# Kernel tuning notes

Measured on AMD Instinct MI355X. Metric: run time of the kernel, lower is better.

The kernel has to match this reference:

```python
import jax
import jax.numpy as jnp
from jax import lax
import numpy as np

# module hyperparameters (match init_kwargs)
IN_C, OUT_C = 32, 64
K, STRIDE, PAD, DIL = 3, 1, 1, 1
GRID_SIZE, ORDER = 5, 3
GRID_LO, GRID_HI = -1.0, 1.0
SCALE_SPLINE = 1.0
EPS = 1e-8


def _knot_grid():
    # grid = arange(-order, grid_size+order+1) * h + lo ; length = grid_size + 2*order + 1 = 12
    h = (GRID_HI - GRID_LO) / GRID_SIZE
    return jnp.arange(-ORDER, GRID_SIZE + ORDER + 1, dtype=jnp.float32) * h + GRID_LO


def _bspline_bases(x):
    """Cox-de Boor recursion. x: (N, P) -> bases: (N, P, GRID_SIZE+ORDER)."""
    grid = _knot_grid()
    xe = x[..., None]  # (N, P, 1)
    bases = ((xe >= grid[:-1]) & (xe < grid[1:])).astype(x.dtype)  # (N, P, 11)
    for k in range(1, ORDER + 1):
        left_den = jnp.maximum(grid[k:-1] - grid[:-(k + 1)], EPS)
        right_den = jnp.maximum(grid[k + 1:] - grid[1:-k], EPS)
        bases = ((xe - grid[:-(k + 1)]) / left_den * bases[..., :-1]
                 + (grid[k + 1:] - xe) / right_den * bases[..., 1:])
    return bases  # (N, P, 8)


def setup_inputs() -> dict:
    key = jax.random.key(0)
    k1, k2, k3 = jax.random.split(key, 3)
    x = jax.random.normal(k1, (4, IN_C, 56, 56), dtype=jnp.float32)
    base_weight = jax.random.normal(k2, (OUT_C, IN_C, K, K), dtype=jnp.float32) * 0.05
    spline_weight = jax.random.normal(k3, (OUT_C, IN_C * K * K, GRID_SIZE + ORDER), dtype=jnp.float32) * 0.05
    spline_scaler = jnp.ones((OUT_C,), dtype=jnp.float32)
    return {"x": x, "base_weight": base_weight,
            "spline_weight": spline_weight, "spline_scaler": spline_scaler}


def reference(x, base_weight, spline_weight, spline_scaler):
    B, C, H, W = x.shape
    pad = [(PAD, PAD), (PAD, PAD)]
    # base path: conv2d -> SiLU
    base_conv = lax.conv_general_dilated(
        x, base_weight, window_strides=(STRIDE, STRIDE), padding=pad,
        rhs_dilation=(DIL, DIL), dimension_numbers=("NCHW", "OIHW", "NCHW"))
    base_out = jax.nn.silu(base_conv)

    # unfold: (B, C*K*K, oh, ow) with torch Unfold channel ordering (c, kh, kw)
    patches = lax.conv_general_dilated_patches(
        x, filter_shape=(K, K), window_strides=(STRIDE, STRIDE), padding=pad,
        rhs_dilation=(DIL, DIL))
    oh, ow = patches.shape[2], patches.shape[3]
    num_patches = oh * ow
    # (B*num_patches, C*K*K)
    pf = patches.reshape(B, C * K * K, num_patches).transpose(0, 2, 1).reshape(-1, C * K * K)

    bases = _bspline_bases(pf)  # (N, P, F)
    # contract patch-dim and basis-dim against spline weights
    spl = jnp.einsum("npf,opf->no", bases, spline_weight) * spline_scaler  # (N, O)
    spl = spl.reshape(B, num_patches, OUT_C).transpose(0, 2, 1).reshape(B, OUT_C, oh, ow)
    return base_out + SCALE_SPLINE * spl
```

## Files before the change

### kernel.cpp

```cpp
#include <hip/hip_runtime.h>
#include <math.h>


typedef __attribute__((ext_vector_type(8))) short bf16x8;
typedef __attribute__((ext_vector_type(4))) float f32x4;

#define MFMA(a, b, c) __builtin_amdgcn_mfma_f32_16x16x32_bf16((a), (b), (c), 0, 0, 0)

__device__ __forceinline__ unsigned short f2bf(float f) {
    unsigned u = __builtin_bit_cast(unsigned, f);
    u = (u + 0x7fffu + ((u >> 16) & 1u)) >> 16;
    return (unsigned short)u;
}

__device__ __forceinline__ void eval_bases(float v, float bs[8]) {
    #pragma unroll
    for (int i = 0; i < 8; ++i) bs[i] = 0.0f;
    float t = (v + 2.2f) * 2.5f;
    if (t >= 0.0f && t < 11.0f) {
        int j = (int)t;
        if (j > 10) j = 10;
        float knot = (float)(j - 3) * 0.4f - 1.0f;
        float u  = (v - knot) * 2.5f;
        float um = 1.0f - u;
        float u2 = u * u, u3 = u2 * u;
        const float s6 = 1.0f / 6.0f;
        float w0 = um * um * um * s6;
        float w1 = (3.0f * u3 - 6.0f * u2 + 4.0f) * s6;
        float w2 = (-3.0f * u3 + 3.0f * u2 + 3.0f * u + 1.0f) * s6;
        float w3 = u3 * s6;
        int i0 = j - 3;
        if (i0 >= 0)               bs[i0]     = w0;
        if (i0 + 1 >= 0 && i0 < 7) bs[i0 + 1] = w1;
        if (i0 + 2 >= 0 && i0 < 6) bs[i0 + 2] = w2;
        if (i0 + 3 <= 7)           bs[i0 + 3] = w3;
    }
}

__global__ __launch_bounds__(256)
void cvt_weights_kernel(const float* __restrict__ ws, const float* __restrict__ wb,
                        unsigned short* __restrict__ wsb, unsigned short* __restrict__ wbb) {
    int i = blockIdx.x * 256 + threadIdx.x;
    if (i < 147456) {
        wsb[i] = f2bf(ws[i]);
    } else {
        int j = i - 147456;
        if (j < 18432) wbb[j] = f2bf(wb[j]);
    }
}

__global__ __launch_bounds__(256)
void kan_mfma_kernel(const float* __restrict__ x,
                     const float* __restrict__ sc,
                     const unsigned short* __restrict__ wsb,
                     const unsigned short* __restrict__ wbb,
                     float* __restrict__ out) {
    __shared__ unsigned short smem[26496];
    unsigned short* sb    = smem;
    unsigned short* sx    = smem + 15360;
    unsigned short* patch = smem + 17280;

    const int tid = threadIdx.x;
    const int bx  = blockIdx.x;
    const int b   = bx / 98;
    const int r   = bx - b * 98;
    const int ty  = r / 7;
    const int tx  = r - ty * 7;
    const int h0  = ty * 4, w0 = tx * 8;

    for (int i = tid; i < 1920; i += 256) {
        int c  = i / 60;
        int hp = i - c * 60;
        int hy = hp / 10;
        int hx = hp - hy * 10;
        int hh = h0 + hy - 1, ww = w0 + hx - 1;
        float v = 0.0f;
        if ((unsigned)hh < 56u && (unsigned)ww < 56u)
            v = x[((b * 32 + c) * 56 + hh) * 56 + ww];
        float bs[8];
        eval_bases(v, bs);
        bf16x8 pk;
        #pragma unroll
        for (int j2 = 0; j2 < 8; ++j2) pk[j2] = (short)f2bf(bs[j2]);
        *reinterpret_cast<bf16x8*>(&sb[i * 8]) = pk;
        sx[i] = f2bf(v);
    }
    __syncthreads();

    {
        int m  = tid >> 3;
        int c0 = (tid & 7) * 4;
        int py = m >> 3, px = m & 7;
        const unsigned short* rsx = &sx[c0 * 60 + py * 10 + px];
        unsigned short* wp = &patch[m * 288 + c0 * 9];
        #pragma unroll
        for (int cc = 0; cc < 4; ++cc)
            #pragma unroll
            for (int kh = 0; kh < 3; ++kh)
                #pragma unroll
                for (int kw = 0; kw < 3; ++kw)
                    wp[cc * 9 + kh * 3 + kw] = rsx[cc * 60 + kh * 10 + kw];
    }
    __syncthreads();

    const int lane = tid & 63;
    const int wv   = tid >> 6;
    const int col  = lane & 15;
    const int q    = lane >> 4;
    const int m0   = col;
    const int py0  = m0 >> 3, px0 = m0 & 7;
    const int oc   = wv * 16 + col;

    f32x4 accS0 = {0.f,0.f,0.f,0.f}, accS1 = {0.f,0.f,0.f,0.f};
    f32x4 accB0 = {0.f,0.f,0.f,0.f}, accB1 = {0.f,0.f,0.f,0.f};

    int aoff[9];
    #pragma unroll
    for (int u = 0; u < 9; ++u) {
        int t4  = 4 * u + q;
        int dc  = t4 / 9;
        int tap = t4 - dc * 9;
        int kh  = tap / 3;
        int kw  = tap - kh * 3;
        aoff[u] = (dc * 60 + (py0 + kh) * 10 + (px0 + kw)) * 8;
    }

    const unsigned short* wBp = wsb + (oc * 288 + q) * 8;
    int gbase = 0;
    for (int g = 0; g < 8; ++g) {
        #pragma unroll
        for (int u = 0; u < 9; ++u) {
            bf16x8 a0 = *reinterpret_cast<const bf16x8*>(&sb[gbase + aoff[u]]);
            bf16x8 a1 = *reinterpret_cast<const bf16x8*>(&sb[gbase + aoff[u] + 160]);
            bf16x8 bw = *reinterpret_cast<const bf16x8*>(wBp + g * 288 + u * 32);
            accS0 = MFMA(a0, bw, accS0);
            accS1 = MFMA(a1, bw, accS1);
        }
        gbase += 1920;
    }

    {
        const unsigned short* ap = &patch[m0 * 288 + q * 8];
        const unsigned short* bp = wbb + oc * 288 + q * 8;
        #pragma unroll
        for (int ks = 0; ks < 9; ++ks) {
            bf16x8 a0 = *reinterpret_cast<const bf16x8*>(ap + ks * 32);
            bf16x8 a1 = *reinterpret_cast<const bf16x8*>(ap + ks * 32 + 4608);
            bf16x8 bw = *reinterpret_cast<const bf16x8*>(bp + ks * 32);
            accB0 = MFMA(a0, bw, accB0);
            accB1 = MFMA(a1, bw, accB1);
        }
    }

    const float scv = sc[oc];
    float* obase = out + ((b * 64 + oc) * 56) * 56;
    #pragma unroll
    for (int mt = 0; mt < 2; ++mt) {
        f32x4 aB = mt ? accB1 : accB0;
        f32x4 aS = mt ? accS1 : accS0;
        int py  = mt * 2 + (q >> 1);
        int pxb = (q & 1) * 4;
        f32x4 res;
        #pragma unroll
        for (int reg = 0; reg < 4; ++reg) {
            float bv = aB[reg];
            float s  = bv / (1.0f + __expf(-bv));
            res[reg] = s + scv * aS[reg];
        }
        *reinterpret_cast<f32x4*>(&obase[(h0 + py) * 56 + w0 + pxb]) = res;
    }
}

extern "C" void kernel_launch(void* const* d_in, const int* in_sizes, int n_in,
                              void* d_out, int out_size, void* d_ws, size_t ws_size,
                              hipStream_t stream) {
    const float* x  = (const float*)d_in[0];
    const float* wb = (const float*)d_in[1];
    const float* ws = (const float*)d_in[2];
    const float* sc = (const float*)d_in[3];
    float* out = (float*)d_out;

    unsigned short* wsb = (unsigned short*)d_ws;
    unsigned short* wbb = wsb + 147456;

    cvt_weights_kernel<<<648, 256, 0, stream>>>(ws, wb, wsb, wbb);
    kan_mfma_kernel<<<392, 256, 0, stream>>>(x, sc, wsb, wbb, out);
}
```

Measured before the change: 89.53 us.

## Switch to 32x32x16 MFMA with split-K across waves and swizzled weights

Replaces the 16x16x32 MFMA tiling, where each wave covered 16 output channels over all of K, with 32x32x16 MFMAs. Waves are split into two N-halves and two K-halves, and the partial sums are reduced through shared memory before the SiLU and add epilogue. The weight conversion kernel now lays weights out in MFMA lane order, so each lane's B load is one contiguous 16-byte read. The patch buffer row stride is padded to reduce LDS bank conflicts. In exchange it adds an LDS reduction with two extra barriers, and only half the waves run the epilogue.

```diff
diff --git a/kernel.cpp b/kernel.cpp
--- a/kernel.cpp
+++ b/kernel.cpp
@@ -2,10 +2,11 @@
 #include <math.h>
 
 
-typedef __attribute__((ext_vector_type(8))) short bf16x8;
-typedef __attribute__((ext_vector_type(4))) float f32x4;
-
-#define MFMA(a, b, c) __builtin_amdgcn_mfma_f32_16x16x32_bf16((a), (b), (c), 0, 0, 0)
+typedef __attribute__((ext_vector_type(8)))  short bf16x8;
+typedef __attribute__((ext_vector_type(4)))  float f32x4;
+typedef __attribute__((ext_vector_type(16))) float f32x16;
+
+#define MFMA32(a, b, c) __builtin_amdgcn_mfma_f32_32x32x16_bf16((a), (b), (c), 0, 0, 0)
 
 __device__ __forceinline__ unsigned short f2bf(float f) {
     unsigned u = __builtin_bit_cast(unsigned, f);
@@ -38,24 +39,34 @@
 }
 
 __global__ __launch_bounds__(256)
-void cvt_weights_kernel(const float* __restrict__ ws, const float* __restrict__ wb,
-                        unsigned short* __restrict__ wsb, unsigned short* __restrict__ wbb) {
+void cvt_swz_kernel(const float* __restrict__ ws, const float* __restrict__ wb,
+                    unsigned short* __restrict__ wst, unsigned short* __restrict__ wbt) {
     int i = blockIdx.x * 256 + threadIdx.x;
     if (i < 147456) {
-        wsb[i] = f2bf(ws[i]);
+        int j = i & 7, l = (i >> 3) & 63, t = i >> 9;
+        int s = t % 144, nf = t / 144;
+        int oc = nf * 32 + (l & 31);
+        int k  = s * 16 + (l >> 5) * 8 + j;
+        wst[i] = f2bf(ws[oc * 2304 + k]);
     } else {
-        int j = i - 147456;
-        if (j < 18432) wbb[j] = f2bf(wb[j]);
+        int i2 = i - 147456;
+        if (i2 < 18432) {
+            int j = i2 & 7, l = (i2 >> 3) & 63, t = i2 >> 9;
+            int s = t % 18, nf = t / 18;
+            int oc = nf * 32 + (l & 31);
+            int k  = s * 16 + (l >> 5) * 8 + j;
+            wbt[i2] = f2bf(wb[oc * 288 + k]);
+        }
     }
 }
 
 __global__ __launch_bounds__(256)
 void kan_mfma_kernel(const float* __restrict__ x,
                      const float* __restrict__ sc,
-                     const unsigned short* __restrict__ wsb,
-                     const unsigned short* __restrict__ wbb,
+                     const unsigned short* __restrict__ wst,
+                     const unsigned short* __restrict__ wbt,
                      float* __restrict__ out) {
-    __shared__ unsigned short smem[26496];
+    __shared__ unsigned short smem[26752];
     unsigned short* sb    = smem;
     unsigned short* sx    = smem + 15360;
     unsigned short* patch = smem + 17280;
@@ -88,11 +99,10 @@
     __syncthreads();
 
     {
-        int m  = tid >> 3;
+        int m2 = tid >> 3;
         int c0 = (tid & 7) * 4;
-        int py = m >> 3, px = m & 7;
-        const unsigned short* rsx = &sx[c0 * 60 + py * 10 + px];
-        unsigned short* wp = &patch[m * 288 + c0 * 9];
+        const unsigned short* rsx = &sx[c0 * 60 + (m2 >> 3) * 10 + (m2 & 7)];
+        unsigned short* wp = &patch[m2 * 296 + c0 * 9];
         #pragma unroll
         for (int cc = 0; cc < 4; ++cc)
             #pragma unroll
@@ -105,69 +115,90 @@
 
     const int lane = tid & 63;
     const int wv   = tid >> 6;
-    const int col  = lane & 15;
-    const int q    = lane >> 4;
-    const int m0   = col;
-    const int py0  = m0 >> 3, px0 = m0 & 7;
-    const int oc   = wv * 16 + col;
-
-    f32x4 accS0 = {0.f,0.f,0.f,0.f}, accS1 = {0.f,0.f,0.f,0.f};
-    f32x4 accB0 = {0.f,0.f,0.f,0.f}, accB1 = {0.f,0.f,0.f,0.f};
+    const int nf   = wv & 1;
+    const int kh2  = wv >> 1;
+    const int m    = lane & 31;
+    const int kg   = lane >> 5;
+    const int py0  = m >> 3, px0 = m & 7;
+
+    f32x16 accS = {0.f}; f32x16 accB = {0.f};
+    #pragma unroll
+    for (int i = 0; i < 16; ++i) { accS[i] = 0.f; accB[i] = 0.f; }
 
     int aoff[9];
     #pragma unroll
     for (int u = 0; u < 9; ++u) {
-        int t4  = 4 * u + q;
-        int dc  = t4 / 9;
-        int tap = t4 - dc * 9;
+        int t2  = 2 * u + kg;
+        int dc  = t2 / 9;
+        int tap = t2 - dc * 9;
         int kh  = tap / 3;
         int kw  = tap - kh * 3;
         aoff[u] = (dc * 60 + (py0 + kh) * 10 + (px0 + kw)) * 8;
     }
 
-    const unsigned short* wBp = wsb + (oc * 288 + q) * 8;
-    int gbase = 0;
+    const unsigned short* bp = wst + ((nf * 144 + kh2 * 72) * 64 + lane) * 8;
+    int cbase = kh2 * 7680;
     for (int g = 0; g < 8; ++g) {
         #pragma unroll
         for (int u = 0; u < 9; ++u) {
-            bf16x8 a0 = *reinterpret_cast<const bf16x8*>(&sb[gbase + aoff[u]]);
-            bf16x8 a1 = *reinterpret_cast<const bf16x8*>(&sb[gbase + aoff[u] + 160]);
-            bf16x8 bw = *reinterpret_cast<const bf16x8*>(wBp + g * 288 + u * 32);
-            accS0 = MFMA(a0, bw, accS0);
-            accS1 = MFMA(a1, bw, accS1);
-        }
-        gbase += 1920;
+            bf16x8 a = *reinterpret_cast<const bf16x8*>(&sb[cbase + aoff[u]]);
+            bf16x8 bw = *reinterpret_cast<const bf16x8*>(bp + (g * 9 + u) * 512);
+            accS = MFMA32(a, bw, accS);
+        }
+        cbase += 960;
     }
 
     {
-        const unsigned short* ap = &patch[m0 * 288 + q * 8];
-        const unsigned short* bp = wbb + oc * 288 + q * 8;
-        #pragma unroll
-        for (int ks = 0; ks < 9; ++ks) {
-            bf16x8 a0 = *reinterpret_cast<const bf16x8*>(ap + ks * 32);
-            bf16x8 a1 = *reinterpret_cast<const bf16x8*>(ap + ks * 32 + 4608);
-            bf16x8 bw = *reinterpret_cast<const bf16x8*>(bp + ks * 32);
-            accB0 = MFMA(a0, bw, accB0);
-            accB1 = MFMA(a1, bw, accB1);
-        }
-    }
-
-    const float scv = sc[oc];
-    float* obase = out + ((b * 64 + oc) * 56) * 56;
-    #pragma unroll
-    for (int mt = 0; mt < 2; ++mt) {
-        f32x4 aB = mt ? accB1 : accB0;
-        f32x4 aS = mt ? accS1 : accS0;
-        int py  = mt * 2 + (q >> 1);
-        int pxb = (q & 1) * 4;
-        f32x4 res;
-        #pragma unroll
-        for (int reg = 0; reg < 4; ++reg) {
-            float bv = aB[reg];
-            float s  = bv / (1.0f + __expf(-bv));
-            res[reg] = s + scv * aS[reg];
-        }
-        *reinterpret_cast<f32x4*>(&obase[(h0 + py) * 56 + w0 + pxb]) = res;
+        const unsigned short* ap  = &patch[m * 296 + kg * 8];
+        const unsigned short* bbp = wbt + ((nf * 18 + kh2 * 9) * 64 + lane) * 8;
+        #pragma unroll
+        for (int s = 0; s < 9; ++s) {
+            bf16x8 a = *reinterpret_cast<const bf16x8*>(ap + (kh2 * 9 + s) * 16);
+            bf16x8 bw = *reinterpret_cast<const bf16x8*>(bbp + s * 512);
+            accB = MFMA32(a, bw, accB);
+        }
+    }
+
+    __syncthreads();
+    float* red = (float*)smem;
+    if (kh2 == 1) {
+        float* dst = red + (nf * 64 + lane) * 36;
+        #pragma unroll
+        for (int rq = 0; rq < 4; ++rq) {
+            f32x4 vS, vB;
+            #pragma unroll
+            for (int rr = 0; rr < 4; ++rr) { vS[rr] = accS[rq*4+rr]; vB[rr] = accB[rq*4+rr]; }
+            *reinterpret_cast<f32x4*>(dst + rq * 4)      = vS;
+            *reinterpret_cast<f32x4*>(dst + 16 + rq * 4) = vB;
+        }
+    }
+    __syncthreads();
+
+    if (kh2 == 0) {
+        const float* src = red + (nf * 64 + lane) * 36;
+        #pragma unroll
+        for (int rq = 0; rq < 4; ++rq) {
+            f32x4 vS = *reinterpret_cast<const f32x4*>(src + rq * 4);
+            f32x4 vB = *reinterpret_cast<const f32x4*>(src + 16 + rq * 4);
+            #pragma unroll
+            for (int rr = 0; rr < 4; ++rr) { accS[rq*4+rr] += vS[rr]; accB[rq*4+rr] += vB[rr]; }
+        }
+        const int col = lane & 31;
+        const int oc  = nf * 32 + col;
+        const float scv = sc[oc];
+        const int kg5 = lane >> 5;
+        float* ob = out + ((b * 64 + oc) * 56 + h0) * 56 + w0 + 4 * kg5;
+        #pragma unroll
+        for (int rq = 0; rq < 4; ++rq) {
+            f32x4 res;
+            #pragma unroll
+            for (int rr = 0; rr < 4; ++rr) {
+                float bv = accB[rq * 4 + rr];
+                float si = bv / (1.0f + __expf(-bv));
+                res[rr] = si + scv * accS[rq * 4 + rr];
+            }
+            *reinterpret_cast<f32x4*>(ob + rq * 56) = res;
+        }
     }
 }
 
@@ -180,9 +211,9 @@
     const float* sc = (const float*)d_in[3];
     float* out = (float*)d_out;
 
-    unsigned short* wsb = (unsigned short*)d_ws;
-    unsigned short* wbb = wsb + 147456;
-
-    cvt_weights_kernel<<<648, 256, 0, stream>>>(ws, wb, wsb, wbb);
-    kan_mfma_kernel<<<392, 256, 0, stream>>>(x, sc, wsb, wbb, out);
-}
+    unsigned short* wst = (unsigned short*)d_ws;
+    unsigned short* wbt = wst + 147456;
+
+    cvt_swz_kernel<<<648, 256, 0, stream>>>(ws, wb, wst, wbt);
+    kan_mfma_kernel<<<392, 256, 0, stream>>>(x, sc, wst, wbt, out);
+}
```

Result: faster. 78.46 us (-12.4%).
